# Optimization experiments

Hardware: AMD Instinct MI355X
Metric: run time of the kernel (lower is better)

Reference implementation:

```python
import jax, jax.numpy as jnp
import numpy as np

B, T, D, H, E = 2, 1024, 1024, 4096, 8


def setup_inputs() -> dict:
    key = jax.random.key(0)
    ks = jax.random.split(key, 7)
    s = 0.02  # weight init scale
    return {
        "x": jax.random.normal(ks[0], (B, T, D), jnp.float32),
        "gate_w": jax.random.normal(ks[1], (D, E), jnp.float32) * s,
        "gate_b": jnp.zeros((E,), jnp.float32),
        "w1": jax.random.normal(ks[2], (E, D, H), jnp.float32) * s,
        "b1": jnp.zeros((E, H), jnp.float32),
        "w2": jax.random.normal(ks[3], (E, H, D), jnp.float32) * s,
        "b2": jnp.zeros((E, D), jnp.float32),
    }


def reference(x, gate_w, gate_b, w1, b1, w2, b2):
    b, t, d = x.shape
    e = gate_w.shape[1]
    xt = x.reshape(b * t, d)                      # [N, D]
    logits = xt @ gate_w + gate_b                 # [N, E]
    probs = jax.nn.softmax(logits, axis=-1)
    top_expert = jnp.argmax(probs, axis=-1)       # [N]
    onehot = jax.nn.one_hot(top_expert, e, dtype=x.dtype)  # [N, E]
    # dense per-expert FFN, then combine via top-1 one-hot (same math as masked dispatch)
    h = jax.nn.gelu(jnp.einsum('nd,edh->enh', xt, w1) + b1[:, None, :], approximate=False)  # [E, N, H]
    y = jnp.einsum('enh,ehd->end', h, w2) + b2[:, None, :]                                  # [E, N, D]
    out = jnp.einsum('end,ne->nd', y, onehot).reshape(b, t, d)
    counts = jnp.sum(onehot, axis=0)              # [E], float
    frac = counts / jnp.maximum(counts.sum(), 1.0)
    aux_loss = jnp.mean((frac - 1.0 / e) ** 2)
    return out, aux_loss
```

## Files before the change

### kernel.cpp

```cpp
#include <hip/hip_runtime.h>
#include <stdint.h>

#define N_TOK 2048
#define DDIM 1024
#define HDIM 4096
#define NEXP 8
#define BM 128
#define MAXT 24
#define PADCAP 3072

#define C_COUNTS 0
#define C_CURSOR 8
#define C_PADOFF 16
#define C_TILECNT 25
#define C_TILE_E 32
#define C_TILE_M0 56
#define C_TILE_ROWS 80
#define C_EXPERT 128
#define C_PERM 2176

#define XG_OFF 32768
#define HG_OFF (XG_OFF + PADCAP*DDIM*2)

typedef float f32x4 __attribute__((ext_vector_type(4)));
typedef short s16x8 __attribute__((ext_vector_type(8)));
typedef unsigned int u32;
typedef u32 u32x2 __attribute__((ext_vector_type(2)));
typedef unsigned short u16;

__device__ __forceinline__ u16 f2bf(float f){
  u32 u = __float_as_uint(f);
  u += 0x7fffu + ((u >> 16) & 1u);
  return (u16)(u >> 16);
}

__device__ __forceinline__ u32 pkbf(float a, float b){
  u32 r; asm("v_cvt_pk_bf16_f32 %0, %1, %2" : "=v"(r) : "v"(a), "v"(b)); return r;
}

__device__ __forceinline__ void gl_lds16(const void* g, void* l){
  __builtin_amdgcn_global_load_lds((const __attribute__((address_space(1))) u32*)g,
                                   (__attribute__((address_space(3))) u32*)l, 16, 0, 0);
}

__global__ __launch_bounds__(256) void gate_kern(
    const float* __restrict__ x, const float* __restrict__ gw,
    const float* __restrict__ gb, int* __restrict__ ctrl)
{
  const int wv = threadIdx.x >> 6, l = threadIdx.x & 63;
  const int n = blockIdx.x * 4 + wv;
  const float* xr = x + (size_t)n * DDIM;
  float acc[NEXP];
  #pragma unroll
  for (int e = 0; e < NEXP; e++) acc[e] = 0.f;
  #pragma unroll 4
  for (int i = 0; i < DDIM/64; i++){
    int k = i*64 + l;
    float xv = xr[k];
    const float* g = gw + (size_t)k * NEXP;
    #pragma unroll
    for (int e = 0; e < NEXP; e++) acc[e] = fmaf(xv, g[e], acc[e]);
  }
  #pragma unroll
  for (int e = 0; e < NEXP; e++){
    #pragma unroll
    for (int off = 32; off > 0; off >>= 1) acc[e] += __shfl_xor(acc[e], off);
  }
  if (l == 0){
    float best = acc[0] + gb[0]; int bi = 0;
    #pragma unroll
    for (int e = 1; e < NEXP; e++){
      float v = acc[e] + gb[e];
      if (v > best){ best = v; bi = e; }
    }
    ctrl[C_EXPERT + n] = bi;
    atomicAdd(&ctrl[C_COUNTS + bi], 1);
  }
}

__global__ void setup_kern(int* __restrict__ ctrl, float* __restrict__ aux_out)
{
  const int t = threadIdx.x;
  for (int i = t; i < PADCAP; i += 256) ctrl[C_PERM + i] = -1;
  if (t == 0){
    int off = 0, tc = 0;
    float aux = 0.f;
    for (int e = 0; e < NEXP; e++){
      int c = ctrl[C_COUNTS + e];
      ctrl[C_PADOFF + e] = off;
      ctrl[C_CURSOR + e] = off;
      int nt = (c + BM - 1) / BM;
      for (int j = 0; j < nt; j++){
        ctrl[C_TILE_E   + tc] = e;
        ctrl[C_TILE_M0  + tc] = off + j*BM;
        ctrl[C_TILE_ROWS+ tc] = min(BM, c - j*BM);
        tc++;
      }
      off += nt * BM;
      float fr = (float)c * (1.f/(float)N_TOK);
      float d = fr - 1.f/(float)NEXP;
      aux += d*d;
    }
    ctrl[C_TILECNT] = tc;
    *aux_out = aux * (1.f/(float)NEXP);
  }
}

__global__ __launch_bounds__(256) void scatter_kern(int* __restrict__ ctrl)
{
  const int n = blockIdx.x * 256 + threadIdx.x;
  const int e = ctrl[C_EXPERT + n];
  const int pos = atomicAdd(&ctrl[C_CURSOR + e], 1);
  ctrl[C_PERM + pos] = n;
}

__global__ __launch_bounds__(256) void xg_kern(
    const float* __restrict__ x, const int* __restrict__ ctrl,
    u16* __restrict__ Xg)
{
  const int slot = blockIdx.x, t = threadIdx.x;
  const int tok = ctrl[C_PERM + slot];
  ushort4 o;
  if (tok >= 0){
    f32x4 v = *(const f32x4*)(x + (size_t)tok*DDIM + t*4);
    o.x = f2bf(v.x); o.y = f2bf(v.y); o.z = f2bf(v.z); o.w = f2bf(v.w);
  } else { o.x = 0; o.y = 0; o.z = 0; o.w = 0; }
  *(ushort4*)(Xg + (size_t)slot*DDIM + t*4) = o;
}

template<int MODE>
__global__ __launch_bounds__(256, 2) void moe_gemm(
    const u16* __restrict__ Ag, const float* __restrict__ W,
    const float* __restrict__ bias, u16* __restrict__ Hg,
    float* __restrict__ outp, const int* __restrict__ ctrl)
{
  constexpr int K   = (MODE==1) ? DDIM : HDIM;
  constexpr int NN  = (MODE==1) ? HDIM : DDIM;
  constexpr int BN  = (MODE==1) ? 128 : 64;
  constexpr int BK  = 64;
  constexpr int BKP = 72;
  constexpr int NF  = BN / 32;
  constexpr int KRP = 4 * (256 / BN);
  constexpr int NPASS = BK / KRP;
  constexpr int WREG  = 4 * NPASS;
  constexpr int NT  = K / BK;

  const int by = blockIdx.y;
  if (by >= ctrl[C_TILECNT]) return;
  const int e    = ctrl[C_TILE_E + by];
  const int m0   = ctrl[C_TILE_M0 + by];
  const int rows = ctrl[C_TILE_ROWS + by];
  const int n0   = blockIdx.x * BN;

  const int tid = threadIdx.x;
  const int w = tid >> 6, l = tid & 63;
  const int wr = w >> 1, wc = w & 1;
  const int lhi = l >> 4, llo = l & 15;

  __shared__ __align__(16) u16 As[2][BM*BK];
  __shared__ __align__(16) u16 Bst[2][BN*BKP];
  __shared__ int perm_s[BM];

  if constexpr (MODE == 2){
    if (tid < BM) perm_s[tid] = ctrl[C_PERM + m0 + tid];
  }

  f32x4 acc[4][NF];
  #pragma unroll
  for (int mf = 0; mf < 4; mf++)
    #pragma unroll
    for (int nf = 0; nf < NF; nf++) acc[mf][nf] = (f32x4){0.f,0.f,0.f,0.f};

  const u16* Abase = Ag + (size_t)m0 * K;
  int arow[4], apos[4];
  #pragma unroll
  for (int i = 0; i < 4; i++){
    int f = i*256 + tid;
    arow[i] = f >> 3;
    apos[i] = (f & 7) ^ (arow[i] & 7);
  }
  u16* adst0 = &As[0][(w*64)*8];
  u16* adst1 = &As[1][(w*64)*8];

  const int wn = tid & (BN-1);
  const int wkg = (tid / BN) & 3;
  const float* Wb = W + (size_t)e * K * NN + n0 + wn;
  float wreg[WREG];

#define STAGE_A(buf, k0) { \
    u16* ad = (buf) ? adst1 : adst0; \
    _Pragma("unroll") \
    for (int i = 0; i < 4; i++) \
      gl_lds16(Abase + (size_t)arow[i]*K + (k0) + apos[i]*8, ad + i*256*8); }

#define LOAD_W(k0) { \
    _Pragma("unroll") \
    for (int g = 0; g < NPASS; g++){ \
      _Pragma("unroll") \
      for (int j = 0; j < 4; j++) \
        wreg[g*4+j] = Wb[(size_t)((k0) + g*KRP + wkg*4 + j) * NN]; } }

#define CVT_W(buf) { \
    _Pragma("unroll") \
    for (int g = 0; g < NPASS; g++){ \
      u32x2 d; d.x = pkbf(wreg[g*4+0], wreg[g*4+1]); \
               d.y = pkbf(wreg[g*4+2], wreg[g*4+3]); \
      *(u32x2*)&Bst[buf][wn*BKP + g*KRP + wkg*4] = d; } }

#define COMPUTE(buf) { \
    _Pragma("unroll") \
    for (int kk = 0; kk < 2; kk++){ \
      s16x8 a[4], b[NF]; \
      _Pragma("unroll") \
      for (int mf = 0; mf < 4; mf++){ \
        int row = wr*64 + mf*16 + llo; \
        int pos = ((kk<<2) | lhi) ^ (row & 7); \
        a[mf] = *(const s16x8*)&As[buf][row*BK + pos*8]; } \
      _Pragma("unroll") \
      for (int nf = 0; nf < NF; nf++){ \
        int col = wc*(BN/2) + nf*16 + llo; \
        b[nf] = *(const s16x8*)&Bst[buf][col*BKP + kk*32 + lhi*8]; } \
      _Pragma("unroll") \
      for (int mf = 0; mf < 4; mf++) \
        _Pragma("unroll") \
        for (int nf = 0; nf < NF; nf++) \
          acc[mf][nf] = __builtin_amdgcn_mfma_f32_16x16x32_bf16(a[mf], b[nf], acc[mf][nf], 0, 0, 0); } }

  STAGE_A(0, 0);
  LOAD_W(0);
  CVT_W(0);
  __syncthreads();

  int cur = 0;
  for (int t = 0; t < NT; t++){
    const int k0n = (t+1)*BK;
    if (t+1 < NT){ STAGE_A(cur^1, k0n); LOAD_W(k0n); }
    COMPUTE(cur);
    if (t+1 < NT){ CVT_W(cur^1); }
    __syncthreads();
    cur ^= 1;
  }

  if constexpr (MODE == 1){
    const float* bp = bias + (size_t)e*NN + n0;
    #pragma unroll
    for (int nf = 0; nf < NF; nf++){
      const int cl = wc*(BN/2) + nf*16 + llo;
      const float bb = bp[cl];
      #pragma unroll
      for (int mf = 0; mf < 4; mf++){
        #pragma unroll
        for (int r = 0; r < 4; r++){
          const int rl = wr*64 + mf*16 + lhi*4 + r;
          float vv = acc[mf][nf][r] + bb;
          float gel = 0.5f * vv * (1.0f + erff(vv * 0.70710678118f));
          Hg[(size_t)(m0+rl)*NN + n0 + cl] = f2bf(gel);
        }
      }
    }
  } else {
    const float* bp = bias + (size_t)e*NN + n0;
    #pragma unroll
    for (int mf = 0; mf < 4; mf++){
      #pragma unroll
      for (int r = 0; r < 4; r++){
        const int rl = wr*64 + mf*16 + lhi*4 + r;
        if (rl < rows){
          const int tok = perm_s[rl];
          #pragma unroll
          for (int nf = 0; nf < NF; nf++){
            const int cl = wc*(BN/2) + nf*16 + llo;
            outp[(size_t)tok*DDIM + n0 + cl] = acc[mf][nf][r] + bp[cl];
          }
        }
      }
    }
  }
#undef STAGE_A
#undef LOAD_W
#undef CVT_W
#undef COMPUTE
}

extern "C" void kernel_launch(void* const* d_in, const int* in_sizes, int n_in,
                              void* d_out, int out_size, void* d_ws, size_t ws_size,
                              hipStream_t stream)
{
  (void)in_sizes; (void)n_in; (void)out_size; (void)ws_size;
  const float* x  = (const float*)d_in[0];
  const float* gw = (const float*)d_in[1];
  const float* gb = (const float*)d_in[2];
  const float* w1 = (const float*)d_in[3];
  const float* b1 = (const float*)d_in[4];
  const float* w2 = (const float*)d_in[5];
  const float* b2 = (const float*)d_in[6];
  float* out = (float*)d_out;
  char* ws = (char*)d_ws;
  int* ctrl = (int*)ws;
  u16* Xg = (u16*)(ws + XG_OFF);
  u16* Hg = (u16*)(ws + HG_OFF);

  hipMemsetAsync(ctrl, 0, 64, stream);
  gate_kern<<<N_TOK/4, 256, 0, stream>>>(x, gw, gb, ctrl);
  setup_kern<<<1, 256, 0, stream>>>(ctrl, out + (size_t)N_TOK*DDIM);
  scatter_kern<<<N_TOK/256, 256, 0, stream>>>(ctrl);
  xg_kern<<<PADCAP, 256, 0, stream>>>(x, ctrl, Xg);
  moe_gemm<1><<<dim3(HDIM/128, MAXT), 256, 0, stream>>>(Xg, w1, b1, Hg, nullptr, ctrl);
  moe_gemm<2><<<dim3(DDIM/64,  MAXT), 256, 0, stream>>>(Hg, w2, b2, nullptr, out, ctrl);
}
```

Baseline: 217.4 us.

## Deepen MoE GEMM pipeline with triple-buffered A, double W registers, manual waitcnt barriers

Reworks the GEMM main loop into a two-stage-ahead software pipeline. A tiles are triple-buffered in LDS, and W prefetch alternates between two register sets. Hand-placed vmcnt waits and raw s_barrier replace __syncthreads, and s_setprio raises priority during the MFMA blocks. For the first GEMM it also halves BK to 32 and raises the occupancy target to 3 blocks per SM, trading fewer MFMAs per sync for more latency hiding. The hard-coded vmcnt counts must match the exact number of outstanding loads, which makes the code fragile.

Result: faster. 211.4 us (-2.8%).

```diff
diff --git a/kernel.cpp b/kernel.cpp
--- a/kernel.cpp
+++ b/kernel.cpp
@@ -129,7 +129,7 @@
 }
 
 template<int MODE>
-__global__ __launch_bounds__(256, 2) void moe_gemm(
+__global__ __launch_bounds__(256, (MODE==1) ? 3 : 2) void moe_gemm(
     const u16* __restrict__ Ag, const float* __restrict__ W,
     const float* __restrict__ bias, u16* __restrict__ Hg,
     float* __restrict__ outp, const int* __restrict__ ctrl)
@@ -137,9 +137,12 @@
   constexpr int K   = (MODE==1) ? DDIM : HDIM;
   constexpr int NN  = (MODE==1) ? HDIM : DDIM;
   constexpr int BN  = (MODE==1) ? 128 : 64;
-  constexpr int BK  = 64;
-  constexpr int BKP = 72;
+  constexpr int BK  = (MODE==1) ? 32 : 64;
+  constexpr int BKP = (MODE==1) ? 40 : 72;
   constexpr int NF  = BN / 32;
+  constexpr int CPR = BK / 8;
+  constexpr int AVM = BK / 16;
+  constexpr int NKK = BK / 32;
   constexpr int KRP = 4 * (256 / BN);
   constexpr int NPASS = BK / KRP;
   constexpr int WREG  = 4 * NPASS;
@@ -157,7 +160,7 @@
   const int wr = w >> 1, wc = w & 1;
   const int lhi = l >> 4, llo = l & 15;
 
-  __shared__ __align__(16) u16 As[2][BM*BK];
+  __shared__ __align__(16) u16 As[3][BM*BK];
   __shared__ __align__(16) u16 Bst[2][BN*BKP];
   __shared__ int perm_s[BM];
 
@@ -172,73 +175,89 @@
     for (int nf = 0; nf < NF; nf++) acc[mf][nf] = (f32x4){0.f,0.f,0.f,0.f};
 
   const u16* Abase = Ag + (size_t)m0 * K;
-  int arow[4], apos[4];
+  int arow[AVM], apos[AVM];
   #pragma unroll
-  for (int i = 0; i < 4; i++){
+  for (int i = 0; i < AVM; i++){
     int f = i*256 + tid;
-    arow[i] = f >> 3;
-    apos[i] = (f & 7) ^ (arow[i] & 7);
-  }
-  u16* adst0 = &As[0][(w*64)*8];
-  u16* adst1 = &As[1][(w*64)*8];
+    arow[i] = f / CPR;
+    apos[i] = (f & (CPR-1)) ^ (arow[i] & (CPR-1));
+  }
 
   const int wn = tid & (BN-1);
   const int wkg = (tid / BN) & 3;
   const float* Wb = W + (size_t)e * K * NN + n0 + wn;
-  float wreg[WREG];
+  float wregA[WREG], wregB[WREG];
+
+#define WAITV(N) asm volatile("s_waitcnt vmcnt(" #N ")" ::: "memory")
+#define WAIT_PIPE() do { if constexpr (MODE==1) WAITV(18); else WAITV(20); } while(0)
+#define PIPE_BAR() do { asm volatile("s_waitcnt lgkmcnt(0)" ::: "memory"); \
+    __builtin_amdgcn_sched_barrier(0); \
+    __builtin_amdgcn_s_barrier(); \
+    __builtin_amdgcn_sched_barrier(0); } while(0)
 
 #define STAGE_A(buf, k0) { \
-    u16* ad = (buf) ? adst1 : adst0; \
+    u16* ad = &As[buf][(w*64)*8]; \
     _Pragma("unroll") \
-    for (int i = 0; i < 4; i++) \
+    for (int i = 0; i < AVM; i++) \
       gl_lds16(Abase + (size_t)arow[i]*K + (k0) + apos[i]*8, ad + i*256*8); }
 
-#define LOAD_W(k0) { \
+#define LOAD_W(dst, k0) { \
     _Pragma("unroll") \
     for (int g = 0; g < NPASS; g++){ \
       _Pragma("unroll") \
       for (int j = 0; j < 4; j++) \
-        wreg[g*4+j] = Wb[(size_t)((k0) + g*KRP + wkg*4 + j) * NN]; } }
-
-#define CVT_W(buf) { \
+        dst[g*4+j] = Wb[(size_t)((k0) + g*KRP + wkg*4 + j) * NN]; } }
+
+#define CVT_W(buf, src) { \
     _Pragma("unroll") \
     for (int g = 0; g < NPASS; g++){ \
-      u32x2 d; d.x = pkbf(wreg[g*4+0], wreg[g*4+1]); \
-               d.y = pkbf(wreg[g*4+2], wreg[g*4+3]); \
+      u32x2 d; d.x = pkbf(src[g*4+0], src[g*4+1]); \
+               d.y = pkbf(src[g*4+2], src[g*4+3]); \
       *(u32x2*)&Bst[buf][wn*BKP + g*KRP + wkg*4] = d; } }
 
-#define COMPUTE(buf) { \
+#define COMPUTE(abuf, bbuf) { \
+    __builtin_amdgcn_s_setprio(1); \
     _Pragma("unroll") \
-    for (int kk = 0; kk < 2; kk++){ \
+    for (int kk = 0; kk < NKK; kk++){ \
       s16x8 a[4], b[NF]; \
       _Pragma("unroll") \
       for (int mf = 0; mf < 4; mf++){ \
         int row = wr*64 + mf*16 + llo; \
-        int pos = ((kk<<2) | lhi) ^ (row & 7); \
-        a[mf] = *(const s16x8*)&As[buf][row*BK + pos*8]; } \
+        int pos = ((kk<<2) | lhi) ^ (row & (CPR-1)); \
+        a[mf] = *(const s16x8*)&As[abuf][row*BK + pos*8]; } \
       _Pragma("unroll") \
       for (int nf = 0; nf < NF; nf++){ \
         int col = wc*(BN/2) + nf*16 + llo; \
-        b[nf] = *(const s16x8*)&Bst[buf][col*BKP + kk*32 + lhi*8]; } \
+        b[nf] = *(const s16x8*)&Bst[bbuf][col*BKP + kk*32 + lhi*8]; } \
       _Pragma("unroll") \
       for (int mf = 0; mf < 4; mf++) \
         _Pragma("unroll") \
         for (int nf = 0; nf < NF; nf++) \
-          acc[mf][nf] = __builtin_amdgcn_mfma_f32_16x16x32_bf16(a[mf], b[nf], acc[mf][nf], 0, 0, 0); } }
-
+          acc[mf][nf] = __builtin_amdgcn_mfma_f32_16x16x32_bf16(a[mf], b[nf], acc[mf][nf], 0, 0, 0); } \
+    __builtin_amdgcn_s_setprio(0); }
+
+#define ITER(tt, LD, CV) { \
+    if ((tt)+2 < NT){ \
+      LOAD_W(LD, ((tt)+2)*BK); \
+      STAGE_A(((tt)+2)%3, ((tt)+2)*BK); \
+    } \
+    COMPUTE((tt)%3, (tt)&1); \
+    if ((tt)+2 < NT){ WAIT_PIPE(); } else { WAITV(0); } \
+    if ((tt)+1 < NT){ CVT_W(((tt)+1)&1, CV); } \
+    PIPE_BAR(); }
+
+  LOAD_W(wregA, 0);
   STAGE_A(0, 0);
-  LOAD_W(0);
-  CVT_W(0);
-  __syncthreads();
-
-  int cur = 0;
-  for (int t = 0; t < NT; t++){
-    const int k0n = (t+1)*BK;
-    if (t+1 < NT){ STAGE_A(cur^1, k0n); LOAD_W(k0n); }
-    COMPUTE(cur);
-    if (t+1 < NT){ CVT_W(cur^1); }
-    __syncthreads();
-    cur ^= 1;
+  LOAD_W(wregB, BK);
+  STAGE_A(1, BK);
+  WAIT_PIPE();
+  CVT_W(0, wregA);
+  PIPE_BAR();
+
+  #pragma unroll 1
+  for (int t = 0; t < NT; t += 2){
+    ITER(t,   wregA, wregB);
+    ITER(t+1, wregB, wregA);
   }
 
   if constexpr (MODE == 1){
@@ -276,10 +295,14 @@
       }
     }
   }
+#undef WAITV
+#undef WAIT_PIPE
+#undef PIPE_BAR
 #undef STAGE_A
 #undef LOAD_W
 #undef CVT_W
 #undef COMPUTE
+#undef ITER
 }
 
 extern "C" void kernel_launch(void* const* d_in, const int* in_sizes, int n_in,
```

## Stage fp32 weights directly to LDS via async loads, convert at MFMA read

Applied to the files above, without the earlier changes.

Instead of loading fp32 weights into registers, converting them to bf16 and writing a transposed copy into LDS, the GEMM now uses global_load_lds to copy raw fp32 weight tiles straight into swizzled LDS. The bf16 packing happens when B fragments are read from LDS before each MFMA. For the first GEMM the K tile is halved to 32 so the larger fp32 LDS buffers fit, and occupancy is raised to 3 blocks per SM. The intent is to free registers and overlap weight loads asynchronously, at the cost of more strided LDS reads and repeated conversion work inside the compute loop.

New measurement: 207.9 us. 1.05x faster.

```diff
diff --git a/kernel.cpp b/kernel.cpp
--- a/kernel.cpp
+++ b/kernel.cpp
@@ -25,7 +25,6 @@
 typedef float f32x4 __attribute__((ext_vector_type(4)));
 typedef short s16x8 __attribute__((ext_vector_type(8)));
 typedef unsigned int u32;
-typedef u32 u32x2 __attribute__((ext_vector_type(2)));
 typedef unsigned short u16;
 
 __device__ __forceinline__ u16 f2bf(float f){
@@ -129,21 +128,22 @@
 }
 
 template<int MODE>
-__global__ __launch_bounds__(256, 2) void moe_gemm(
+__global__ __launch_bounds__(256, (MODE==1) ? 3 : 2) void moe_gemm(
     const u16* __restrict__ Ag, const float* __restrict__ W,
     const float* __restrict__ bias, u16* __restrict__ Hg,
     float* __restrict__ outp, const int* __restrict__ ctrl)
 {
-  constexpr int K   = (MODE==1) ? DDIM : HDIM;
-  constexpr int NN  = (MODE==1) ? HDIM : DDIM;
-  constexpr int BN  = (MODE==1) ? 128 : 64;
-  constexpr int BK  = 64;
-  constexpr int BKP = 72;
-  constexpr int NF  = BN / 32;
-  constexpr int KRP = 4 * (256 / BN);
-  constexpr int NPASS = BK / KRP;
-  constexpr int WREG  = 4 * NPASS;
-  constexpr int NT  = K / BK;
+  constexpr int K    = (MODE==1) ? DDIM : HDIM;
+  constexpr int NN   = (MODE==1) ? HDIM : DDIM;
+  constexpr int BN   = (MODE==1) ? 128 : 64;
+  constexpr int BK   = (MODE==1) ? 32 : 64;
+  constexpr int NF   = BN / 32;
+  constexpr int NKK  = BK / 32;
+  constexpr int CPR  = BK / 8;
+  constexpr int AVM  = (BM*BK)/(256*8);
+  constexpr int BCPR = BN / 4;
+  constexpr int BVM  = (BK*BN)/(256*4);
+  constexpr int NT   = K / BK;
 
   const int by = blockIdx.y;
   if (by >= ctrl[C_TILECNT]) return;
@@ -157,8 +157,8 @@
   const int wr = w >> 1, wc = w & 1;
   const int lhi = l >> 4, llo = l & 15;
 
-  __shared__ __align__(16) u16 As[2][BM*BK];
-  __shared__ __align__(16) u16 Bst[2][BN*BKP];
+  __shared__ __align__(16) u16   As[2][BM*BK];
+  __shared__ __align__(16) float Bs[2][BK*BN];
   __shared__ int perm_s[BM];
 
   if constexpr (MODE == 2){
@@ -172,71 +172,73 @@
     for (int nf = 0; nf < NF; nf++) acc[mf][nf] = (f32x4){0.f,0.f,0.f,0.f};
 
   const u16* Abase = Ag + (size_t)m0 * K;
-  int arow[4], apos[4];
-  #pragma unroll
-  for (int i = 0; i < 4; i++){
+  int arow[AVM], apos[AVM];
+  #pragma unroll
+  for (int i = 0; i < AVM; i++){
     int f = i*256 + tid;
-    arow[i] = f >> 3;
-    apos[i] = (f & 7) ^ (arow[i] & 7);
-  }
-  u16* adst0 = &As[0][(w*64)*8];
-  u16* adst1 = &As[1][(w*64)*8];
-
-  const int wn = tid & (BN-1);
-  const int wkg = (tid / BN) & 3;
-  const float* Wb = W + (size_t)e * K * NN + n0 + wn;
-  float wreg[WREG];
+    arow[i] = f / CPR;
+    apos[i] = (f & (CPR-1)) ^ (arow[i] & (CPR-1));
+  }
+  const float* Wb = W + (size_t)e * K * NN + n0;
+  int brow[BVM], bpos[BVM];
+  #pragma unroll
+  for (int i = 0; i < BVM; i++){
+    int f = i*256 + tid;
+    brow[i] = f / BCPR;
+    bpos[i] = (f % BCPR) ^ (((brow[i] >> 3) & 1) << 2);
+  }
+
+  const int col0 = wc*(BN/2) + llo;
+  const int bswz = (lhi & 1) << 2;
 
 #define STAGE_A(buf, k0) { \
-    u16* ad = (buf) ? adst1 : adst0; \
+    u16* ad = &As[buf][(w*64)*8]; \
     _Pragma("unroll") \
-    for (int i = 0; i < 4; i++) \
+    for (int i = 0; i < AVM; i++) \
       gl_lds16(Abase + (size_t)arow[i]*K + (k0) + apos[i]*8, ad + i*256*8); }
 
-#define LOAD_W(k0) { \
+#define STAGE_B(buf, k0) { \
+    float* bd = &Bs[buf][(w*64)*4]; \
     _Pragma("unroll") \
-    for (int g = 0; g < NPASS; g++){ \
-      _Pragma("unroll") \
-      for (int j = 0; j < 4; j++) \
-        wreg[g*4+j] = Wb[(size_t)((k0) + g*KRP + wkg*4 + j) * NN]; } }
-
-#define CVT_W(buf) { \
-    _Pragma("unroll") \
-    for (int g = 0; g < NPASS; g++){ \
-      u32x2 d; d.x = pkbf(wreg[g*4+0], wreg[g*4+1]); \
-               d.y = pkbf(wreg[g*4+2], wreg[g*4+3]); \
-      *(u32x2*)&Bst[buf][wn*BKP + g*KRP + wkg*4] = d; } }
+    for (int i = 0; i < BVM; i++) \
+      gl_lds16(Wb + (size_t)((k0) + brow[i])*NN + bpos[i]*4, bd + i*256*4); }
 
 #define COMPUTE(buf) { \
     _Pragma("unroll") \
-    for (int kk = 0; kk < 2; kk++){ \
-      s16x8 a[4], b[NF]; \
+    for (int kk = 0; kk < NKK; kk++){ \
+      s16x8 a[4]; \
       _Pragma("unroll") \
       for (int mf = 0; mf < 4; mf++){ \
         int row = wr*64 + mf*16 + llo; \
-        int pos = ((kk<<2) | lhi) ^ (row & 7); \
+        int pos = ((kk<<2) | lhi) ^ (row & (CPR-1)); \
         a[mf] = *(const s16x8*)&As[buf][row*BK + pos*8]; } \
       _Pragma("unroll") \
       for (int nf = 0; nf < NF; nf++){ \
-        int col = wc*(BN/2) + nf*16 + llo; \
-        b[nf] = *(const s16x8*)&Bst[buf][col*BKP + kk*32 + lhi*8]; } \
-      _Pragma("unroll") \
-      for (int mf = 0; mf < 4; mf++) \
+        const int col = col0 + nf*16; \
+        const float* bp_ = &Bs[buf][(kk*32 + lhi*8)*BN + \
+                                    ((((col) >> 2) ^ bswz) << 2) + ((col) & 3)]; \
+        union { u32 u[4]; s16x8 v; } bb_; \
+        bb_.u[0] = pkbf(bp_[0*BN], bp_[1*BN]); \
+        bb_.u[1] = pkbf(bp_[2*BN], bp_[3*BN]); \
+        bb_.u[2] = pkbf(bp_[4*BN], bp_[5*BN]); \
+        bb_.u[3] = pkbf(bp_[6*BN], bp_[7*BN]); \
         _Pragma("unroll") \
-        for (int nf = 0; nf < NF; nf++) \
-          acc[mf][nf] = __builtin_amdgcn_mfma_f32_16x16x32_bf16(a[mf], b[nf], acc[mf][nf], 0, 0, 0); } }
+        for (int mf = 0; mf < 4; mf++) \
+          acc[mf][nf] = __builtin_amdgcn_mfma_f32_16x16x32_bf16(a[mf], bb_.v, acc[mf][nf], 0, 0, 0); \
+      } } }
 
   STAGE_A(0, 0);
-  LOAD_W(0);
-  CVT_W(0);
+  STAGE_B(0, 0);
   __syncthreads();
 
   int cur = 0;
+  #pragma unroll 1
   for (int t = 0; t < NT; t++){
-    const int k0n = (t+1)*BK;
-    if (t+1 < NT){ STAGE_A(cur^1, k0n); LOAD_W(k0n); }
+    if (t+1 < NT){
+      STAGE_A(cur^1, (t+1)*BK);
+      STAGE_B(cur^1, (t+1)*BK);
+    }
     COMPUTE(cur);
-    if (t+1 < NT){ CVT_W(cur^1); }
     __syncthreads();
     cur ^= 1;
   }
@@ -277,8 +279,7 @@
     }
   }
 #undef STAGE_A
-#undef LOAD_W
-#undef CVT_W
+#undef STAGE_B
 #undef COMPUTE
 }
 
```
